# Performance work log

Measured on AMD Instinct MI355X. Metric: run time of the kernel, lower is better.

## Reference

```python
import jax, jax.numpy as jnp
import numpy as np
from jax import lax

V, E, H, MLP, NCLS = 50000, 100, 100, 300, 3
B, T, C = 256, 128, 255


def _lstm_dir(x, Wih, Whh, bih, bhh, reverse):
    # x: [T, B, E]; PyTorch gate order i, f, g, o
    Bsz = x.shape[1]
    h0 = jnp.zeros((Bsz, H), x.dtype)
    c0 = jnp.zeros((Bsz, H), x.dtype)

    def step(carry, xt):
        h, c = carry
        gates = xt @ Wih.T + h @ Whh.T + (bih + bhh)  # [B, 4H]
        i, f, g, o = jnp.split(gates, 4, axis=-1)
        c = jax.nn.sigmoid(f) * c + jax.nn.sigmoid(i) * jnp.tanh(g)
        h = jax.nn.sigmoid(o) * jnp.tanh(c)
        return (h, c), h

    _, hs = lax.scan(step, (h0, c0), x, reverse=reverse)
    return hs  # [T, B, H]


def setup_inputs() -> dict:
    key = jax.random.key(0)
    ks = jax.random.split(key, 16)
    s_e = 1.0 / np.sqrt(H)
    inp = {
        "x": jax.random.randint(ks[0], (B, T), 0, V),
        "paths": jax.random.randint(ks[1], (B, C, 3), 0, T),
        "emb": jax.random.normal(ks[2], (V, E), jnp.float32),
        "Wih_f": jax.random.uniform(ks[3], (4 * H, E), jnp.float32, -s_e, s_e),
        "Whh_f": jax.random.uniform(ks[4], (4 * H, H), jnp.float32, -s_e, s_e),
        "bih_f": jax.random.uniform(ks[5], (4 * H,), jnp.float32, -s_e, s_e),
        "bhh_f": jax.random.uniform(ks[6], (4 * H,), jnp.float32, -s_e, s_e),
        "Wih_b": jax.random.uniform(ks[7], (4 * H, E), jnp.float32, -s_e, s_e),
        "Whh_b": jax.random.uniform(ks[8], (4 * H, H), jnp.float32, -s_e, s_e),
        "bih_b": jax.random.uniform(ks[9], (4 * H,), jnp.float32, -s_e, s_e),
        "bhh_b": jax.random.uniform(ks[10], (4 * H,), jnp.float32, -s_e, s_e),
        "W1": jax.random.normal(ks[11], (6 * H, MLP), jnp.float32) * 0.05,
        "b1": jnp.zeros((MLP,), jnp.float32),
        "W2": jax.random.normal(ks[12], (MLP, NCLS), jnp.float32) * 0.05,
        "b2": jnp.zeros((NCLS,), jnp.float32),
    }
    return inp


def reference(x, paths, emb, Wih_f, Whh_f, bih_f, bhh_f, Wih_b, Whh_b, bih_b, bhh_b, W1, b1, W2, b2):
    # embedding lookup (dropout is eval-mode identity)
    xe = emb[x]                      # [B, T, E]
    xe = jnp.transpose(xe, (1, 0, 2))  # [T, B, E] (seq-major like packed LSTM)
    hf = _lstm_dir(xe, Wih_f, Whh_f, bih_f, bhh_f, reverse=False)
    hb = _lstm_dir(xe, Wih_b, Whh_b, bih_b, bhh_b, reverse=True)
    h = jnp.concatenate([hf, hb], axis=-1)        # [T, B, 2H]
    hbt = jnp.transpose(h, (1, 0, 2))             # [B, T, 2H]
    # gather 3 positions per configuration; index -1 -> zero vector
    idx = jnp.clip(paths, 0, T - 1)               # [B, C, 3]
    g = hbt[jnp.arange(hbt.shape[0])[:, None, None], idx]  # [B, C, 3, 2H]
    g = jnp.where((paths >= 0)[..., None], g, 0.0)
    mlp_in = g.reshape(-1, 6 * H)                 # [B*C, 600]
    hdn = jnp.tanh(mlp_in @ W1 + b1)
    return jax.nn.softmax(hdn @ W2 + b2, axis=-1)  # [B*C, 3]
```

## Files before the change

### kernel.cpp

```cpp
#include <hip/hip_runtime.h>

typedef unsigned short u16;
typedef short short8 __attribute__((ext_vector_type(8)));
typedef float f32x4 __attribute__((ext_vector_type(4)));

__device__ __forceinline__ u16 f2b(float x){
  union{float f; unsigned u;} v; v.f = x;
  unsigned r = (v.u + 0x7FFFu + ((v.u >> 16) & 1u)) >> 16;
  return (u16)r;
}
__device__ __forceinline__ float b2f(u16 h){
  union{unsigned u; float f;} v; v.u = ((unsigned)h) << 16; return v.f;
}
__device__ __forceinline__ float sigm(float x){ return 1.0f/(1.0f + __expf(-x)); }
__device__ __forceinline__ float tanh_f(float x){ return 1.0f - 2.0f/(1.0f + __expf(2.0f*x)); }

__global__ void prep_kernel(const int* __restrict__ x, const float* __restrict__ emb,
   const float* __restrict__ Wih_f, const float* __restrict__ Whh_f,
   const float* __restrict__ bih_f, const float* __restrict__ bhh_f,
   const float* __restrict__ Wih_b, const float* __restrict__ Whh_b,
   const float* __restrict__ bih_b, const float* __restrict__ bhh_b,
   const float* __restrict__ W1,
   u16* __restrict__ xe, u16* __restrict__ wc, float* __restrict__ biasC,
   float* __restrict__ whhT, u16* __restrict__ w1b, u16* __restrict__ hbt)
{
  int id = blockIdx.x*256 + threadIdx.x;
  const int N0 = 32768*128;
  const int N1 = 832*128;
  const int N2 = 800;
  const int N3 = 80000;
  const int N4 = 672*320;
  const int N5 = 32768*24;
  if (id < N0){
    int p = id >> 7, k = id & 127;
    float v = 0.f;
    if (k < 100) v = emb[x[p]*100 + k];
    xe[id] = f2b(v);
    return;
  }
  id -= N0;
  if (id < N1){
    int n = id >> 7, k = id & 127;
    float v = 0.f;
    if (k < 100){
      if (n < 400) v = Wih_f[n*100+k];
      else if (n < 800) v = Wih_b[(n-400)*100+k];
    }
    wc[id] = f2b(v);
    return;
  }
  id -= N1;
  if (id < N2){
    biasC[id] = (id < 400) ? (bih_f[id]+bhh_f[id]) : (bih_b[id-400]+bhh_b[id-400]);
    return;
  }
  id -= N2;
  if (id < N3){
    int d = id / 40000; int rem = id - d*40000; int k = rem / 400; int j = rem - k*400;
    const float* W = d ? Whh_b : Whh_f;
    whhT[id] = W[j*100 + k];
    return;
  }
  id -= N3;
  if (id < N4){
    int k = id / 320; int n = id - k*320;
    int seg = k / 224; int wwk = k - seg*224;
    float v = 0.f;
    if (n < 300 && wwk < 200) v = W1[(seg*200 + wwk)*300 + n];
    w1b[n*672 + k] = f2b(v);
    return;
  }
  id -= N4;
  if (id < N5){
    int p = id / 24; int k = id - p*24;
    hbt[p*224 + 200 + k] = 0;
  }
}

__global__ __launch_bounds__(256) void gemm1_kernel(const u16* __restrict__ xe,
    const u16* __restrict__ wc, const float* __restrict__ biasC, u16* __restrict__ inp)
{
  __shared__ __align__(16) u16 As[64*136];
  __shared__ __align__(16) u16 Bs[64*136];
  const int m0 = blockIdx.x*64, n0 = blockIdx.y*64;
  const int tid = threadIdx.x;
  #pragma unroll
  for (int i=0;i<4;i++){
    int f = i*256 + tid;
    int row = f >> 4, c8 = f & 15;
    *(uint4*)&As[row*136 + c8*8] = *(const uint4*)&xe[(m0+row)*128 + c8*8];
    *(uint4*)&Bs[row*136 + c8*8] = *(const uint4*)&wc[(n0+row)*128 + c8*8];
  }
  __syncthreads();
  const int w = tid >> 6, lane = tid & 63, col = lane & 15, quad = lane >> 4;
  f32x4 acc[4];
  #pragma unroll
  for (int nt=0;nt<4;nt++) acc[nt] = (f32x4){0.f,0.f,0.f,0.f};
  #pragma unroll
  for (int kc=0;kc<4;kc++){
    short8 af = *(const short8*)&As[(w*16+col)*136 + kc*32 + quad*8];
    #pragma unroll
    for (int nt=0;nt<4;nt++){
      short8 bfrag = *(const short8*)&Bs[(nt*16+col)*136 + kc*32 + quad*8];
      acc[nt] = __builtin_amdgcn_mfma_f32_16x16x32_bf16(af, bfrag, acc[nt], 0, 0, 0);
    }
  }
  #pragma unroll
  for (int nt=0;nt<4;nt++){
    int n = n0 + nt*16 + col;
    if (n < 800){
      float bs = biasC[n];
      int dir = (n >= 400) ? 1 : 0;
      int j = n - dir*400;
      #pragma unroll
      for (int r=0;r<4;r++){
        int m = m0 + w*16 + quad*4 + r;
        inp[(dir*32768 + m)*400 + j] = f2b(acc[nt][r] + bs);
      }
    }
  }
}

__global__ __launch_bounds__(448, 4) void lstm_kernel(const u16* __restrict__ inp,
    const float* __restrict__ whhT, u16* __restrict__ hbt)
{
  const int cid = blockIdx.x;
  const int b = cid & 255, dir = cid >> 8;
  const int jj = threadIdx.x;
  __shared__ __align__(16) float hs[104];
  __shared__ float act[400];
  float whh[100];
  if (jj < 400){
    const float* wp = whhT + dir*40000 + jj;
    #pragma unroll
    for (int k=0;k<100;k++) whh[k] = wp[k*400];
  }
  if (jj < 104) hs[jj] = 0.f;
  float c = 0.f;
  const u16* ip = inp + (dir*32768 + b*128)*400;
  u16* hp = hbt + b*128*224;
  __syncthreads();
  for (int step=0; step<128; step++){
    int t = dir ? (127-step) : step;
    if (jj < 400){
      float pre = b2f(ip[t*400 + jj]);
      const float4* h4 = (const float4*)hs;
      float a0=0.f,a1=0.f,a2=0.f,a3=0.f;
      #pragma unroll
      for (int kk=0;kk<25;kk++){
        float4 hv = h4[kk];
        a0 = fmaf(whh[4*kk+0], hv.x, a0);
        a1 = fmaf(whh[4*kk+1], hv.y, a1);
        a2 = fmaf(whh[4*kk+2], hv.z, a2);
        a3 = fmaf(whh[4*kk+3], hv.w, a3);
      }
      float xg = pre + ((a0+a1)+(a2+a3));
      act[jj] = (jj >= 200 && jj < 300) ? tanh_f(xg) : sigm(xg);
    }
    __syncthreads();
    if (jj < 100){
      float ig = act[jj], fg = act[100+jj], gg = act[200+jj], og = act[300+jj];
      c = fg*c + ig*gg;
      float hk = og * tanh_f(c);
      hs[jj] = hk;
      hp[t*224 + dir*100 + jj] = f2b(hk);
    }
    __syncthreads();
  }
}

__global__ __launch_bounds__(512) void mlp_kernel(const u16* __restrict__ hbt,
    const u16* __restrict__ w1b, const int* __restrict__ paths,
    const float* __restrict__ b1, const float* __restrict__ W2,
    const float* __restrict__ b2, float* __restrict__ out)
{
  __shared__ __align__(16) u16 As[128*40];
  __shared__ __align__(16) u16 Bs[320*40];
  const int m0 = blockIdx.x*128;
  const int tid = threadIdx.x;
  const int arow = tid >> 2, ac8 = tid & 3;
  const int am = m0 + arow;
  const int ab = am / 255;
  const int w = tid >> 6, lane = tid & 63, col = lane & 15, quad = lane >> 4;
  f32x4 acc[20];
  #pragma unroll
  for (int nt=0;nt<20;nt++) acc[nt] = (f32x4){0.f,0.f,0.f,0.f};
  for (int kc=0;kc<21;kc++){
    __syncthreads();
    for (int f = tid; f < 1280; f += 512){
      int br = f >> 2, bc = f & 3;
      *(uint4*)&Bs[br*40 + bc*8] = *(const uint4*)&w1b[br*672 + kc*32 + bc*8];
    }
    int seg = (kc >= 14) ? 2 : (kc >= 7 ? 1 : 0);
    int ko = kc - seg*7;
    int it = paths[am*3 + seg];
    uint4 v = make_uint4(0u,0u,0u,0u);
    if (it >= 0){
      int t = it > 127 ? 127 : it;
      v = *(const uint4*)&hbt[(ab*128 + t)*224 + ko*32 + ac8*8];
    }
    *(uint4*)&As[arow*40 + ac8*8] = v;
    __syncthreads();
    short8 af = *(const short8*)&As[(w*16+col)*40 + quad*8];
    #pragma unroll
    for (int nt=0;nt<20;nt++){
      short8 bfrag = *(const short8*)&Bs[(nt*16+col)*40 + quad*8];
      acc[nt] = __builtin_amdgcn_mfma_f32_16x16x32_bf16(af, bfrag, acc[nt], 0, 0, 0);
    }
  }
  float pz[4][3];
  #pragma unroll
  for (int r=0;r<4;r++){ pz[r][0]=0.f; pz[r][1]=0.f; pz[r][2]=0.f; }
  #pragma unroll
  for (int nt=0;nt<20;nt++){
    int n = nt*16 + col;
    if (n < 300){
      float bb = b1[n];
      float w20 = W2[n*3+0], w21 = W2[n*3+1], w22 = W2[n*3+2];
      #pragma unroll
      for (int r=0;r<4;r++){
        float hdn = tanh_f(acc[nt][r] + bb);
        pz[r][0] = fmaf(hdn, w20, pz[r][0]);
        pz[r][1] = fmaf(hdn, w21, pz[r][1]);
        pz[r][2] = fmaf(hdn, w22, pz[r][2]);
      }
    }
  }
  #pragma unroll
  for (int off=1; off<16; off<<=1){
    #pragma unroll
    for (int r=0;r<4;r++){
      pz[r][0] += __shfl_xor(pz[r][0], off, 64);
      pz[r][1] += __shfl_xor(pz[r][1], off, 64);
      pz[r][2] += __shfl_xor(pz[r][2], off, 64);
    }
  }
  float c0 = b2[0], c1 = b2[1], c2 = b2[2];
  #pragma unroll
  for (int r=0;r<4;r++){
    float z0 = pz[r][0]+c0, z1 = pz[r][1]+c1, z2 = pz[r][2]+c2;
    float mx = fmaxf(z0, fmaxf(z1, z2));
    float e0 = __expf(z0-mx), e1 = __expf(z1-mx), e2 = __expf(z2-mx);
    float inv = 1.0f/(e0+e1+e2);
    if (col < 3){
      float pv = (col==0 ? e0 : (col==1 ? e1 : e2)) * inv;
      out[(m0 + w*16 + quad*4 + r)*3 + col] = pv;
    }
  }
}

extern "C" void kernel_launch(void* const* d_in, const int* in_sizes, int n_in,
                              void* d_out, int out_size, void* d_ws, size_t ws_size,
                              hipStream_t stream)
{
  const int*   x     = (const int*)  d_in[0];
  const int*   paths = (const int*)  d_in[1];
  const float* emb   = (const float*)d_in[2];
  const float* Wih_f = (const float*)d_in[3];
  const float* Whh_f = (const float*)d_in[4];
  const float* bih_f = (const float*)d_in[5];
  const float* bhh_f = (const float*)d_in[6];
  const float* Wih_b = (const float*)d_in[7];
  const float* Whh_b = (const float*)d_in[8];
  const float* bih_b = (const float*)d_in[9];
  const float* bhh_b = (const float*)d_in[10];
  const float* W1    = (const float*)d_in[11];
  const float* b1    = (const float*)d_in[12];
  const float* W2    = (const float*)d_in[13];
  const float* b2    = (const float*)d_in[14];
  float* out = (float*)d_out;

  char* ws = (char*)d_ws;
  u16*   xe    = (u16*)  (ws + 0);
  u16*   wc    = (u16*)  (ws + 8388608);
  float* biasC = (float*)(ws + 8601600);
  float* whhT  = (float*)(ws + 8604800);
  u16*   w1b   = (u16*)  (ws + 8924800);
  u16*   inp   = (u16*)  (ws + 9354880);
  u16*   hbt   = (u16*)  (ws + 61783680);

  const int prep_total = 32768*128 + 832*128 + 800 + 80000 + 672*320 + 32768*24;
  prep_kernel<<<(prep_total + 255)/256, 256, 0, stream>>>(
      x, emb, Wih_f, Whh_f, bih_f, bhh_f, Wih_b, Whh_b, bih_b, bhh_b, W1,
      xe, wc, biasC, whhT, w1b, hbt);
  gemm1_kernel<<<dim3(512, 13), 256, 0, stream>>>(xe, wc, biasC, inp);
  lstm_kernel<<<512, 448, 0, stream>>>(inp, whhT, hbt);
  mlp_kernel<<<510, 512, 0, stream>>>(hbt, w1b, paths, b1, W2, b2, out);
}
```

Before: 362.5 us.

## Batch LSTM recurrence over 16 sequences per block using split-bf16 MFMA

The LSTM recurrence now runs in 32 blocks, each handling 16 batch sequences in one direction. The h@Whh product uses MFMA with hi/lo bf16 splitting of both weights and hidden state to keep near-fp32 accuracy. The hidden state is double-buffered in shared memory, which leaves one barrier per step instead of two. The input projection is written in a layout that matches the MFMA fragments, and the embedding gather is fused into gemm1, dropping the separate xe buffer. The cost is far fewer blocks for the serial loop, so only 32 CUs are busy, and three MFMA passes per step.

```diff
diff --git a/kernel.cpp b/kernel.cpp
--- a/kernel.cpp
+++ b/kernel.cpp
@@ -1,6 +1,7 @@
 #include <hip/hip_runtime.h>
 
 typedef unsigned short u16;
+typedef unsigned int u32;
 typedef short short8 __attribute__((ext_vector_type(8)));
 typedef float f32x4 __attribute__((ext_vector_type(4)));
 
@@ -15,30 +16,21 @@
 __device__ __forceinline__ float sigm(float x){ return 1.0f/(1.0f + __expf(-x)); }
 __device__ __forceinline__ float tanh_f(float x){ return 1.0f - 2.0f/(1.0f + __expf(2.0f*x)); }
 
-__global__ void prep_kernel(const int* __restrict__ x, const float* __restrict__ emb,
-   const float* __restrict__ Wih_f, const float* __restrict__ Whh_f,
+__global__ void prep_kernel(const float* __restrict__ Wih_f, const float* __restrict__ Whh_f,
    const float* __restrict__ bih_f, const float* __restrict__ bhh_f,
    const float* __restrict__ Wih_b, const float* __restrict__ Whh_b,
    const float* __restrict__ bih_b, const float* __restrict__ bhh_b,
    const float* __restrict__ W1,
-   u16* __restrict__ xe, u16* __restrict__ wc, float* __restrict__ biasC,
-   float* __restrict__ whhT, u16* __restrict__ w1b, u16* __restrict__ hbt)
+   u16* __restrict__ wc, float* __restrict__ biasC,
+   u16* __restrict__ whhH, u16* __restrict__ whhL,
+   u16* __restrict__ w1b, u16* __restrict__ hbt)
 {
   int id = blockIdx.x*256 + threadIdx.x;
-  const int N0 = 32768*128;
   const int N1 = 832*128;
   const int N2 = 800;
-  const int N3 = 80000;
+  const int N3 = 2*448*128;
   const int N4 = 672*320;
   const int N5 = 32768*24;
-  if (id < N0){
-    int p = id >> 7, k = id & 127;
-    float v = 0.f;
-    if (k < 100) v = emb[x[p]*100 + k];
-    xe[id] = f2b(v);
-    return;
-  }
-  id -= N0;
   if (id < N1){
     int n = id >> 7, k = id & 127;
     float v = 0.f;
@@ -56,9 +48,17 @@
   }
   id -= N2;
   if (id < N3){
-    int d = id / 40000; int rem = id - d*40000; int k = rem / 400; int j = rem - k*400;
-    const float* W = d ? Whh_b : Whh_f;
-    whhT[id] = W[j*100 + k];
+    int d = id / 57344; int rem = id - d*57344;
+    int p = rem >> 7, k = rem & 127;
+    int gg = p / 112; int j = p - gg*112;
+    float v = 0.f;
+    if (j < 100 && k < 100){
+      const float* W = d ? Whh_b : Whh_f;
+      v = W[(gg*100 + j)*100 + k];
+    }
+    u16 hi = f2b(v);
+    whhH[id] = hi;
+    whhL[id] = f2b(v - b2f(hi));
     return;
   }
   id -= N3;
@@ -77,18 +77,30 @@
   }
 }
 
-__global__ __launch_bounds__(256) void gemm1_kernel(const u16* __restrict__ xe,
-    const u16* __restrict__ wc, const float* __restrict__ biasC, u16* __restrict__ inp)
+__global__ __launch_bounds__(256) void gemm1_kernel(const int* __restrict__ x,
+    const float* __restrict__ emb, const u16* __restrict__ wc,
+    const float* __restrict__ biasC, u16* __restrict__ inpP)
 {
   __shared__ __align__(16) u16 As[64*136];
   __shared__ __align__(16) u16 Bs[64*136];
   const int m0 = blockIdx.x*64, n0 = blockIdx.y*64;
   const int tid = threadIdx.x;
+  {
+    int row = tid >> 2, kq = tid & 3;
+    const float* er = emb + (long long)x[m0+row]*100;
+    #pragma unroll
+    for (int kk=0;kk<8;kk++){
+      int k = kq*32 + kk*4;
+      float4 v = make_float4(0.f,0.f,0.f,0.f);
+      if (k < 100) v = *(const float4*)&er[k];
+      ushort4 s; s.x=f2b(v.x); s.y=f2b(v.y); s.z=f2b(v.z); s.w=f2b(v.w);
+      *(ushort4*)&As[row*136 + k] = s;
+    }
+  }
   #pragma unroll
   for (int i=0;i<4;i++){
     int f = i*256 + tid;
     int row = f >> 4, c8 = f & 15;
-    *(uint4*)&As[row*136 + c8*8] = *(const uint4*)&xe[(m0+row)*128 + c8*8];
     *(uint4*)&Bs[row*136 + c8*8] = *(const uint4*)&wc[(n0+row)*128 + c8*8];
   }
   __syncthreads();
@@ -105,67 +117,139 @@
       acc[nt] = __builtin_amdgcn_mfma_f32_16x16x32_bf16(af, bfrag, acc[nt], 0, 0, 0);
     }
   }
+  const int mrow0 = m0 + w*16 + quad*4;
+  const int b = mrow0 >> 7, t0 = mrow0 & 127;
+  const int ghi = b >> 4, m16 = b & 15;
+  const int q2 = m16 >> 2, r2 = m16 & 3;
   #pragma unroll
   for (int nt=0;nt<4;nt++){
     int n = n0 + nt*16 + col;
     if (n < 800){
       float bs = biasC[n];
       int dir = (n >= 400) ? 1 : 0;
-      int j = n - dir*400;
+      int gi = n - dir*400;
+      int gg = gi / 100;
+      int j = gi - gg*100;
+      int wL = j >> 4, colL = j & 15;
+      int g = dir*16 + ghi;
+      size_t base = (((size_t)(g*128 + t0)*7 + wL)*4 + gg)*256 + (q2*16 + colL)*4 + r2;
       #pragma unroll
       for (int r=0;r<4;r++){
-        int m = m0 + w*16 + quad*4 + r;
-        inp[(dir*32768 + m)*400 + j] = f2b(acc[nt][r] + bs);
+        inpP[base + (size_t)r*7168] = f2b(acc[nt][r] + bs);
       }
     }
   }
 }
 
-__global__ __launch_bounds__(448, 4) void lstm_kernel(const u16* __restrict__ inp,
-    const float* __restrict__ whhT, u16* __restrict__ hbt)
-{
-  const int cid = blockIdx.x;
-  const int b = cid & 255, dir = cid >> 8;
-  const int jj = threadIdx.x;
-  __shared__ __align__(16) float hs[104];
-  __shared__ float act[400];
-  float whh[100];
-  if (jj < 400){
-    const float* wp = whhT + dir*40000 + jj;
-    #pragma unroll
-    for (int k=0;k<100;k++) whh[k] = wp[k*400];
-  }
-  if (jj < 104) hs[jj] = 0.f;
-  float c = 0.f;
-  const u16* ip = inp + (dir*32768 + b*128)*400;
-  u16* hp = hbt + b*128*224;
+__global__ __launch_bounds__(448, 2) void lstm_kernel(const u16* __restrict__ inpP,
+    const u16* __restrict__ whhH, const u16* __restrict__ whhL, u16* __restrict__ hbt)
+{
+  __shared__ __align__(16) u16 hs[2][2][16][136];
+  const int g = blockIdx.x;
+  const int dir = g >> 4, gh = g & 15;
+  const int tid = threadIdx.x;
+  const int w = tid >> 6, lane = tid & 63, col = lane & 15, q = lane >> 4;
+  for (int i = tid; i < 4352; i += 448) ((u32*)hs)[i] = 0u;
+  short8 bh[4][4], bl[4][4];
+  {
+    int p = w*16 + col;
+    #pragma unroll
+    for (int gg=0;gg<4;gg++)
+      #pragma unroll
+      for (int kc=0;kc<4;kc++){
+        size_t off = (size_t)(dir*448 + gg*112 + p)*128 + kc*32 + q*8;
+        bh[gg][kc] = *(const short8*)&whhH[off];
+        bl[gg][kc] = *(const short8*)&whhL[off];
+      }
+  }
+  float c[4] = {0.f,0.f,0.f,0.f};
+  const int j = w*16 + col;
+  const bool jv = (j < 100);
+  const u16* ip_lane = inpP + (size_t)g*128*7168 + w*1024 + lane*4;
+  u16* hbr[4];
+  int hswr[4];
+  #pragma unroll
+  for (int r=0;r<4;r++){
+    hbr[r] = hbt + (size_t)(gh*16 + 4*q + r)*28672 + dir*100 + j;
+    hswr[r] = (4*q + r)*68 + w*8 + (col>>1);
+  }
+  const int hsrd = col*68 + q*4;
+  int cur = 0;
+  int t = dir ? 127 : 0;
+  uint2 pre[4];
   __syncthreads();
+  #pragma unroll
+  for (int gg=0;gg<4;gg++) pre[gg] = *(const uint2*)&ip_lane[(size_t)t*7168 + gg*256];
+
   for (int step=0; step<128; step++){
-    int t = dir ? (127-step) : step;
-    if (jj < 400){
-      float pre = b2f(ip[t*400 + jj]);
-      const float4* h4 = (const float4*)hs;
-      float a0=0.f,a1=0.f,a2=0.f,a3=0.f;
-      #pragma unroll
-      for (int kk=0;kk<25;kk++){
-        float4 hv = h4[kk];
-        a0 = fmaf(whh[4*kk+0], hv.x, a0);
-        a1 = fmaf(whh[4*kk+1], hv.y, a1);
-        a2 = fmaf(whh[4*kk+2], hv.z, a2);
-        a3 = fmaf(whh[4*kk+3], hv.w, a3);
+    t = dir ? (127-step) : step;
+    short8 ah[4], al[4];
+    const u32* hb32 = (const u32*)hs + cur*2176 + hsrd;
+    #pragma unroll
+    for (int kc=0;kc<4;kc++){
+      ah[kc] = *(const short8*)(hb32 + kc*16);
+      al[kc] = *(const short8*)(hb32 + 1088 + kc*16);
+    }
+    f32x4 acc[4];
+    #pragma unroll
+    for (int gg=0;gg<4;gg++) acc[gg] = (f32x4){0.f,0.f,0.f,0.f};
+    #pragma unroll
+    for (int kc=0;kc<4;kc++)
+      #pragma unroll
+      for (int gg=0;gg<4;gg++)
+        acc[gg] = __builtin_amdgcn_mfma_f32_16x16x32_bf16(ah[kc], bh[gg][kc], acc[gg], 0, 0, 0);
+    #pragma unroll
+    for (int kc=0;kc<4;kc++)
+      #pragma unroll
+      for (int gg=0;gg<4;gg++)
+        acc[gg] = __builtin_amdgcn_mfma_f32_16x16x32_bf16(al[kc], bh[gg][kc], acc[gg], 0, 0, 0);
+    #pragma unroll
+    for (int kc=0;kc<4;kc++)
+      #pragma unroll
+      for (int gg=0;gg<4;gg++)
+        acc[gg] = __builtin_amdgcn_mfma_f32_16x16x32_bf16(ah[kc], bl[gg][kc], acc[gg], 0, 0, 0);
+    float pr[4][4];
+    #pragma unroll
+    for (int gg=0;gg<4;gg++){
+      union{u32 u; float f;} v;
+      v.u = pre[gg].x << 16;         pr[gg][0] = v.f;
+      v.u = pre[gg].x & 0xffff0000u; pr[gg][1] = v.f;
+      v.u = pre[gg].y << 16;         pr[gg][2] = v.f;
+      v.u = pre[gg].y & 0xffff0000u; pr[gg][3] = v.f;
+    }
+    if (step < 127){
+      int tn = dir ? (126-step) : (step+1);
+      #pragma unroll
+      for (int gg=0;gg<4;gg++) pre[gg] = *(const uint2*)&ip_lane[(size_t)tn*7168 + gg*256];
+    }
+    float h[4];
+    #pragma unroll
+    for (int r=0;r<4;r++){
+      float xi = acc[0][r] + pr[0][r];
+      float xf = acc[1][r] + pr[1][r];
+      float xg = acc[2][r] + pr[2][r];
+      float xo = acc[3][r] + pr[3][r];
+      float fi = sigm(xi), ff = sigm(xf), gv = tanh_f(xg), fo = sigm(xo);
+      c[r] = ff*c[r] + fi*gv;
+      h[r] = fo * tanh_f(c[r]);
+    }
+    u32* hw32 = (u32*)hs + (cur^1)*2176;
+    #pragma unroll
+    for (int r=0;r<4;r++){
+      u16 hb = f2b(h[r]);
+      float lo = h[r] - b2f(hb);
+      u32 my = (u32)hb | ((u32)f2b(lo) << 16);
+      u32 other = __shfl_xor((int)my, 1, 64);
+      if ((col & 1) == 0){
+        u32 pk_hi = (my & 0xffffu) | ((other & 0xffffu) << 16);
+        u32 pk_lo = (my >> 16) | (other & 0xffff0000u);
+        hw32[hswr[r]] = pk_hi;
+        hw32[1088 + hswr[r]] = pk_lo;
+        if (jv) *(u32*)(hbr[r] + (size_t)t*224) = pk_hi;
       }
-      float xg = pre + ((a0+a1)+(a2+a3));
-      act[jj] = (jj >= 200 && jj < 300) ? tanh_f(xg) : sigm(xg);
     }
     __syncthreads();
-    if (jj < 100){
-      float ig = act[jj], fg = act[100+jj], gg = act[200+jj], og = act[300+jj];
-      c = fg*c + ig*gg;
-      float hk = og * tanh_f(c);
-      hs[jj] = hk;
-      hp[t*224 + dir*100 + jj] = f2b(hk);
-    }
-    __syncthreads();
+    cur ^= 1;
   }
 }
 
@@ -196,8 +280,8 @@
     int it = paths[am*3 + seg];
     uint4 v = make_uint4(0u,0u,0u,0u);
     if (it >= 0){
-      int t = it > 127 ? 127 : it;
-      v = *(const uint4*)&hbt[(ab*128 + t)*224 + ko*32 + ac8*8];
+      int tt = it > 127 ? 127 : it;
+      v = *(const uint4*)&hbt[(ab*128 + tt)*224 + ko*32 + ac8*8];
     }
     *(uint4*)&As[arow*40 + ac8*8] = v;
     __syncthreads();
@@ -271,19 +355,19 @@
   float* out = (float*)d_out;
 
   char* ws = (char*)d_ws;
-  u16*   xe    = (u16*)  (ws + 0);
-  u16*   wc    = (u16*)  (ws + 8388608);
-  float* biasC = (float*)(ws + 8601600);
-  float* whhT  = (float*)(ws + 8604800);
-  u16*   w1b   = (u16*)  (ws + 8924800);
-  u16*   inp   = (u16*)  (ws + 9354880);
-  u16*   hbt   = (u16*)  (ws + 61783680);
-
-  const int prep_total = 32768*128 + 832*128 + 800 + 80000 + 672*320 + 32768*24;
+  u16*   wc    = (u16*)  (ws + 0);
+  float* biasC = (float*)(ws + 212992);
+  u16*   whhH  = (u16*)  (ws + 216192);
+  u16*   whhL  = (u16*)  (ws + 445568);
+  u16*   w1b   = (u16*)  (ws + 674944);
+  u16*   inpP  = (u16*)  (ws + 1105024);
+  u16*   hbt   = (u16*)  (ws + 59825280);
+
+  const int prep_total = 832*128 + 800 + 2*448*128 + 672*320 + 32768*24;
   prep_kernel<<<(prep_total + 255)/256, 256, 0, stream>>>(
-      x, emb, Wih_f, Whh_f, bih_f, bhh_f, Wih_b, Whh_b, bih_b, bhh_b, W1,
-      xe, wc, biasC, whhT, w1b, hbt);
-  gemm1_kernel<<<dim3(512, 13), 256, 0, stream>>>(xe, wc, biasC, inp);
-  lstm_kernel<<<512, 448, 0, stream>>>(inp, whhT, hbt);
+      Wih_f, Whh_f, bih_f, bhh_f, Wih_b, Whh_b, bih_b, bhh_b, W1,
+      wc, biasC, whhH, whhL, w1b, hbt);
+  gemm1_kernel<<<dim3(512, 13), 256, 0, stream>>>(x, emb, wc, biasC, inpP);
+  lstm_kernel<<<32, 448, 0, stream>>>(inpP, whhH, whhL, hbt);
   mlp_kernel<<<510, 512, 0, stream>>>(hbt, w1b, paths, b1, W2, b2, out);
 }
```

New measurement: 566.6 us. 1.56x slower.

## Fuse embedding gather into gemm1, interleave gates, batch two sequences per LSTM block

Applied to the files above, without the earlier changes.

The embedding lookup moves out of the prep kernel into gemm1, which gathers emb rows and converts them to bf16 in shared memory, removing the xe round trip through global memory. Gate columns are interleaved (unit*4+gate) in both whhT and the precomputed input buffer. Each LSTM block now handles two batch rows with double-buffered hidden state, so the recurrent weights are reused across both rows. Gate combination uses wave shuffles instead of a shared-memory act array, cutting per-step barriers from two to one, and the next step's input is prefetched. In exchange only 256 LSTM blocks are launched, so there is less parallelism across the GPU.

```diff
diff --git a/kernel.cpp b/kernel.cpp
--- a/kernel.cpp
+++ b/kernel.cpp
@@ -1,6 +1,7 @@
 #include <hip/hip_runtime.h>
 
 typedef unsigned short u16;
+typedef unsigned int u32;
 typedef short short8 __attribute__((ext_vector_type(8)));
 typedef float f32x4 __attribute__((ext_vector_type(4)));
 
@@ -15,30 +16,22 @@
 __device__ __forceinline__ float sigm(float x){ return 1.0f/(1.0f + __expf(-x)); }
 __device__ __forceinline__ float tanh_f(float x){ return 1.0f - 2.0f/(1.0f + __expf(2.0f*x)); }
 
-__global__ void prep_kernel(const int* __restrict__ x, const float* __restrict__ emb,
-   const float* __restrict__ Wih_f, const float* __restrict__ Whh_f,
+#define BAR_LDS() asm volatile("s_waitcnt lgkmcnt(0)\n\ts_barrier" ::: "memory")
+
+__global__ void prep_kernel(const float* __restrict__ Wih_f, const float* __restrict__ Whh_f,
    const float* __restrict__ bih_f, const float* __restrict__ bhh_f,
    const float* __restrict__ Wih_b, const float* __restrict__ Whh_b,
    const float* __restrict__ bih_b, const float* __restrict__ bhh_b,
    const float* __restrict__ W1,
-   u16* __restrict__ xe, u16* __restrict__ wc, float* __restrict__ biasC,
+   u16* __restrict__ wc, float* __restrict__ biasC,
    float* __restrict__ whhT, u16* __restrict__ w1b, u16* __restrict__ hbt)
 {
   int id = blockIdx.x*256 + threadIdx.x;
-  const int N0 = 32768*128;
   const int N1 = 832*128;
   const int N2 = 800;
   const int N3 = 80000;
   const int N4 = 672*320;
   const int N5 = 32768*24;
-  if (id < N0){
-    int p = id >> 7, k = id & 127;
-    float v = 0.f;
-    if (k < 100) v = emb[x[p]*100 + k];
-    xe[id] = f2b(v);
-    return;
-  }
-  id -= N0;
   if (id < N1){
     int n = id >> 7, k = id & 127;
     float v = 0.f;
@@ -56,9 +49,11 @@
   }
   id -= N2;
   if (id < N3){
-    int d = id / 40000; int rem = id - d*40000; int k = rem / 400; int j = rem - k*400;
+    int d = id / 40000; int rem = id - d*40000;
+    int k = rem / 400; int t = rem - k*400;
+    int u = t >> 2, gg = t & 3;
     const float* W = d ? Whh_b : Whh_f;
-    whhT[id] = W[j*100 + k];
+    whhT[id] = W[(gg*100 + u)*100 + k];
     return;
   }
   id -= N3;
@@ -77,18 +72,30 @@
   }
 }
 
-__global__ __launch_bounds__(256) void gemm1_kernel(const u16* __restrict__ xe,
-    const u16* __restrict__ wc, const float* __restrict__ biasC, u16* __restrict__ inp)
+__global__ __launch_bounds__(256) void gemm1_kernel(const int* __restrict__ x,
+    const float* __restrict__ emb, const u16* __restrict__ wc,
+    const float* __restrict__ biasC, u16* __restrict__ inp)
 {
   __shared__ __align__(16) u16 As[64*136];
   __shared__ __align__(16) u16 Bs[64*136];
   const int m0 = blockIdx.x*64, n0 = blockIdx.y*64;
   const int tid = threadIdx.x;
+  {
+    int row = tid >> 2, kq = tid & 3;
+    const float* er = emb + (long long)x[m0+row]*100;
+    #pragma unroll
+    for (int kk=0;kk<8;kk++){
+      int k = kq*32 + kk*4;
+      float4 v = make_float4(0.f,0.f,0.f,0.f);
+      if (k < 100) v = *(const float4*)&er[k];
+      ushort4 s; s.x=f2b(v.x); s.y=f2b(v.y); s.z=f2b(v.z); s.w=f2b(v.w);
+      *(ushort4*)&As[row*136 + k] = s;
+    }
+  }
   #pragma unroll
   for (int i=0;i<4;i++){
     int f = i*256 + tid;
     int row = f >> 4, c8 = f & 15;
-    *(uint4*)&As[row*136 + c8*8] = *(const uint4*)&xe[(m0+row)*128 + c8*8];
     *(uint4*)&Bs[row*136 + c8*8] = *(const uint4*)&wc[(n0+row)*128 + c8*8];
   }
   __syncthreads();
@@ -105,67 +112,96 @@
       acc[nt] = __builtin_amdgcn_mfma_f32_16x16x32_bf16(af, bfrag, acc[nt], 0, 0, 0);
     }
   }
+  const int mrow0 = m0 + w*16 + quad*4;
   #pragma unroll
   for (int nt=0;nt<4;nt++){
     int n = n0 + nt*16 + col;
     if (n < 800){
       float bs = biasC[n];
       int dir = (n >= 400) ? 1 : 0;
-      int j = n - dir*400;
+      int gi = n - dir*400;
+      int gg = gi / 100;
+      int uu = gi - gg*100;
+      int jn = uu*4 + gg;
+      u16* op = inp + ((size_t)(dir*32768 + mrow0))*400 + jn;
       #pragma unroll
-      for (int r=0;r<4;r++){
-        int m = m0 + w*16 + quad*4 + r;
-        inp[(dir*32768 + m)*400 + j] = f2b(acc[nt][r] + bs);
-      }
-    }
-  }
-}
-
-__global__ __launch_bounds__(448, 4) void lstm_kernel(const u16* __restrict__ inp,
+      for (int r=0;r<4;r++) op[(size_t)r*400] = f2b(acc[nt][r] + bs);
+    }
+  }
+}
+
+__global__ __launch_bounds__(448) void lstm_kernel(const u16* __restrict__ inp,
     const float* __restrict__ whhT, u16* __restrict__ hbt)
 {
-  const int cid = blockIdx.x;
-  const int b = cid & 255, dir = cid >> 8;
+  __shared__ __align__(16) float hs[2][208];
+  const int bid = blockIdx.x;
+  const int dir = bid >> 7, i2 = bid & 127;
+  const int b0 = i2*2;
   const int jj = threadIdx.x;
-  __shared__ __align__(16) float hs[104];
-  __shared__ float act[400];
+  const int tg = jj & 3, u = jj >> 2;
+  for (int k = jj; k < 416; k += 448) ((float*)hs)[k] = 0.f;
   float whh[100];
-  if (jj < 400){
+  const bool act = (jj < 400);
+  if (act){
     const float* wp = whhT + dir*40000 + jj;
     #pragma unroll
     for (int k=0;k<100;k++) whh[k] = wp[k*400];
   }
-  if (jj < 104) hs[jj] = 0.f;
-  float c = 0.f;
-  const u16* ip = inp + (dir*32768 + b*128)*400;
-  u16* hp = hbt + b*128*224;
+  const u16* ip0 = inp + ((size_t)(dir*32768 + b0*128))*400 + jj;
+  const u16* ip1 = ip0 + 51200;
+  u16* hb0 = hbt + (size_t)(b0*128)*224 + dir*100 + u;
+  u16* hb1 = hb0 + 28672;
+  float cA = 0.f, cB = 0.f;
+  int cur = 0;
   __syncthreads();
+  int t0 = dir ? 127 : 0;
+  u16 preA = 0, preB = 0;
+  if (act){ preA = ip0[(size_t)t0*400]; preB = ip1[(size_t)t0*400]; }
   for (int step=0; step<128; step++){
     int t = dir ? (127-step) : step;
-    if (jj < 400){
-      float pre = b2f(ip[t*400 + jj]);
-      const float4* h4 = (const float4*)hs;
-      float a0=0.f,a1=0.f,a2=0.f,a3=0.f;
+    if (act){
+      float pA = b2f(preA), pB = b2f(preB);
+      if (step < 127){
+        int tn = dir ? (126-step) : (step+1);
+        preA = ip0[(size_t)tn*400];
+        preB = ip1[(size_t)tn*400];
+      }
+      const float4* h4 = (const float4*)hs[cur];
+      float a0=0.f, a1=0.f, d0=0.f, d1=0.f;
       #pragma unroll
-      for (int kk=0;kk<25;kk++){
-        float4 hv = h4[kk];
-        a0 = fmaf(whh[4*kk+0], hv.x, a0);
-        a1 = fmaf(whh[4*kk+1], hv.y, a1);
-        a2 = fmaf(whh[4*kk+2], hv.z, a2);
-        a3 = fmaf(whh[4*kk+3], hv.w, a3);
-      }
-      float xg = pre + ((a0+a1)+(a2+a3));
-      act[jj] = (jj >= 200 && jj < 300) ? tanh_f(xg) : sigm(xg);
-    }
-    __syncthreads();
-    if (jj < 100){
-      float ig = act[jj], fg = act[100+jj], gg = act[200+jj], og = act[300+jj];
-      c = fg*c + ig*gg;
-      float hk = og * tanh_f(c);
-      hs[jj] = hk;
-      hp[t*224 + dir*100 + jj] = f2b(hk);
-    }
-    __syncthreads();
+      for (int kk=0;kk<50;kk+=2){
+        float4 v0 = h4[kk], v1 = h4[kk+1];
+        a0 = fmaf(whh[2*kk+0], v0.x, a0);  d0 = fmaf(whh[2*kk+0], v0.y, d0);
+        a1 = fmaf(whh[2*kk+1], v0.z, a1);  d1 = fmaf(whh[2*kk+1], v0.w, d1);
+        a0 = fmaf(whh[2*kk+2], v1.x, a0);  d0 = fmaf(whh[2*kk+2], v1.y, d0);
+        a1 = fmaf(whh[2*kk+3], v1.z, a1);  d1 = fmaf(whh[2*kk+3], v1.w, d1);
+      }
+      float xA = pA + a0 + a1;
+      float xB = pB + d0 + d1;
+      float pA1 = __shfl_xor(xA, 1, 64), pA2 = __shfl_xor(xA, 2, 64), pA3 = __shfl_xor(pA1, 2, 64);
+      float pB1 = __shfl_xor(xB, 1, 64), pB2 = __shfl_xor(xB, 2, 64), pB3 = __shfl_xor(pB1, 2, 64);
+      const bool s1 = (tg & 1), s2 = (tg & 2);
+      float hA, hB;
+      {
+        float q0 = s1? pA1:xA, q1 = s1? xA:pA1, q2 = s1? pA3:pA2, q3 = s1? pA2:pA3;
+        float gi = s2? q2:q0, gf = s2? q3:q1, gv = s2? q0:q2, go = s2? q1:q3;
+        cA = sigm(gf)*cA + sigm(gi)*tanh_f(gv);
+        hA = sigm(go)*tanh_f(cA);
+      }
+      {
+        float q0 = s1? pB1:xB, q1 = s1? xB:pB1, q2 = s1? pB3:pB2, q3 = s1? pB2:pB3;
+        float gi = s2? q2:q0, gf = s2? q3:q1, gv = s2? q0:q2, go = s2? q1:q3;
+        cB = sigm(gf)*cB + sigm(gi)*tanh_f(gv);
+        hB = sigm(go)*tanh_f(cB);
+      }
+      if (tg == 0){
+        *(float2*)&hs[cur^1][2*u] = make_float2(hA, hB);
+        hb0[(size_t)t*224] = f2b(hA);
+        hb1[(size_t)t*224] = f2b(hB);
+      }
+    }
+    BAR_LDS();
+    cur ^= 1;
   }
 }
 
@@ -196,8 +232,8 @@
     int it = paths[am*3 + seg];
     uint4 v = make_uint4(0u,0u,0u,0u);
     if (it >= 0){
-      int t = it > 127 ? 127 : it;
-      v = *(const uint4*)&hbt[(ab*128 + t)*224 + ko*32 + ac8*8];
+      int tt = it > 127 ? 127 : it;
+      v = *(const uint4*)&hbt[(ab*128 + tt)*224 + ko*32 + ac8*8];
     }
     *(uint4*)&As[arow*40 + ac8*8] = v;
     __syncthreads();
@@ -271,19 +307,18 @@
   float* out = (float*)d_out;
 
   char* ws = (char*)d_ws;
-  u16*   xe    = (u16*)  (ws + 0);
-  u16*   wc    = (u16*)  (ws + 8388608);
-  float* biasC = (float*)(ws + 8601600);
-  float* whhT  = (float*)(ws + 8604800);
-  u16*   w1b   = (u16*)  (ws + 8924800);
-  u16*   inp   = (u16*)  (ws + 9354880);
-  u16*   hbt   = (u16*)  (ws + 61783680);
-
-  const int prep_total = 32768*128 + 832*128 + 800 + 80000 + 672*320 + 32768*24;
+  u16*   wc    = (u16*)  (ws + 0);
+  float* biasC = (float*)(ws + 212992);
+  float* whhT  = (float*)(ws + 216192);
+  u16*   w1b   = (u16*)  (ws + 536192);
+  u16*   inp   = (u16*)  (ws + 966272);
+  u16*   hbt   = (u16*)  (ws + 53395072);
+
+  const int prep_total = 832*128 + 800 + 80000 + 672*320 + 32768*24;
   prep_kernel<<<(prep_total + 255)/256, 256, 0, stream>>>(
-      x, emb, Wih_f, Whh_f, bih_f, bhh_f, Wih_b, Whh_b, bih_b, bhh_b, W1,
-      xe, wc, biasC, whhT, w1b, hbt);
-  gemm1_kernel<<<dim3(512, 13), 256, 0, stream>>>(xe, wc, biasC, inp);
-  lstm_kernel<<<512, 448, 0, stream>>>(inp, whhT, hbt);
+      Wih_f, Whh_f, bih_f, bhh_f, Wih_b, Whh_b, bih_b, bhh_b, W1,
+      wc, biasC, whhT, w1b, hbt);
+  gemm1_kernel<<<dim3(512, 13), 256, 0, stream>>>(x, emb, wc, biasC, inp);
+  lstm_kernel<<<256, 448, 0, stream>>>(inp, whhT, hbt);
   mlp_kernel<<<510, 512, 0, stream>>>(hbt, w1b, paths, b1, W2, b2, out);
 }
```

After: 496.1 us. 1.37x slower.
